# Optimization experiments

Measured on AMD Instinct MI355X. Metric: run time of the kernel, lower is better.

Reference implementation:

```python
import jax, jax.numpy as jnp
import numpy as np
from jax import lax

L = 25            # max_delay (250 // init_spike_step=10, odd)
SIG = 12.0        # max_delay // 2, frozen (requires_grad=False)
BN_EPS = 1e-5
EPS = 1e-7


def _dcls_kernel(W, P):
    # Gaussian interpolation of kernel_count=1 weights onto a dense kernel of size L.
    # W, P: (out, in). Returns (out, in, L).
    grid = jnp.arange(L, dtype=W.dtype) - L // 2          # (L,)
    K = jnp.exp(-0.5 * ((grid[None, None, :] - P[:, :, None]) / SIG) ** 2)
    K = K / (jnp.sum(K, axis=-1, keepdims=True) + EPS)    # normalize over kernel taps
    return W[:, :, None] * K


def _dcls_conv(x_tbc, W, P):
    # x_tbc: (T, B, Cin) -> causal dilated-kernel conv over time -> (T, B, Cout)
    kernel = _dcls_kernel(W, P)                           # (Cout, Cin, L)
    xb = jnp.transpose(x_tbc, (1, 2, 0))                  # (B, Cin, T)
    xb = jnp.pad(xb, ((0, 0), (0, 0), (L - 1, 0)))        # left (causal) padding
    y = lax.conv_general_dilated(xb, kernel, window_strides=(1,), padding='VALID',
                                 dimension_numbers=('NCH', 'OIH', 'NCH'))
    return jnp.transpose(y, (2, 0, 1))                    # (T, B, Cout)


def _bn(x_tbc, gamma, beta):
    # BatchNorm1d with step_mode='m': stats over merged (T, B) per channel.
    mean = jnp.mean(x_tbc, axis=(0, 1))
    var = jnp.var(x_tbc, axis=(0, 1))
    xhat = (x_tbc - mean) * lax.rsqrt(var + BN_EPS)
    return gamma * xhat + beta


def setup_inputs() -> dict:
    key = jax.random.key(0)
    ks = jax.random.split(key, 8)
    B, T, C = 128, 100, 700
    x = jax.random.uniform(ks[0], (B, T, C), dtype=jnp.float32)
    pmax = float(L // 2)
    W1 = jax.random.normal(ks[1], (256, 700), jnp.float32) * (1.0 / np.sqrt(700))
    P1 = jax.random.uniform(ks[2], (256, 700), jnp.float32, minval=-pmax, maxval=pmax)
    W2 = jax.random.normal(ks[3], (256, 256), jnp.float32) * (1.0 / np.sqrt(256))
    P2 = jax.random.uniform(ks[4], (256, 256), jnp.float32, minval=-pmax, maxval=pmax)
    W3 = jax.random.normal(ks[5], (20, 256), jnp.float32) * (1.0 / np.sqrt(256))
    P3 = jax.random.uniform(ks[6], (20, 256), jnp.float32, minval=-pmax, maxval=pmax)
    return {
        'x': x, 'W1': W1, 'P1': P1, 'W2': W2, 'P2': P2, 'W3': W3, 'P3': P3,
        'gamma1': jnp.ones((256,), jnp.float32), 'beta1': jnp.zeros((256,), jnp.float32),
        'gamma2': jnp.ones((256,), jnp.float32), 'beta2': jnp.zeros((256,), jnp.float32),
    }


def reference(x, W1, P1, W2, P2, W3, P3, gamma1, beta1, gamma2, beta2):
    h = jnp.transpose(x, (1, 0, 2))            # (T, B, C)
    h = _dcls_conv(h, W1, P1)                  # (T, B, 256)
    h = jax.nn.relu(_bn(h, gamma1, beta1))     # dropout = identity (eval)
    h = _dcls_conv(h, W2, P2)                  # (T, B, 256)
    h = jax.nn.relu(_bn(h, gamma2, beta2))
    h = _dcls_conv(h, W3, P3)                  # (T, B, 20)
    return jnp.sum(jax.nn.softmax(h, axis=2), axis=0)   # (B, 20)
```

## Files before the change

kernel.cpp:

```cpp
#include <hip/hip_runtime.h>
#include <stdint.h>


#define T_LEN 100
#define B_SZ  128
#define M_ROWS 12800
#define R_RANK 5
#define K_FIR 512

typedef __bf16 v8bf __attribute__((ext_vector_type(8)));
typedef float  v4f  __attribute__((ext_vector_type(4)));
typedef unsigned int uint32;
typedef unsigned short ushort_t;

struct PhiT { float v[25][R_RANK]; };
constexpr double cexp_(double x) {
  double s = 1.0, t = 1.0;
  for (int n = 1; n < 30; ++n) { t = t * x / n; s += t; }
  return s;
}
constexpr PhiT make_phi() {
  PhiT P{};
  for (int tau = 0; tau < 25; ++tau) {
    double u = (tau - 12) / 12.0;
    double g = cexp_(-0.5 * u * u);
    double T0 = 1.0, T1 = u;
    P.v[tau][0] = (float)(g * T0);
    P.v[tau][1] = (float)(g * T1);
    for (int r = 2; r < R_RANK; ++r) {
      double T2 = 2.0 * u * T1 - T0;
      P.v[tau][r] = (float)(g * T2);
      T0 = T1; T1 = T2;
    }
  }
  return P;
}
constexpr PhiT PHI = make_phi();

__device__ __forceinline__ void gl_lds16(const void* g, void* l) {
  __builtin_amdgcn_global_load_lds(
      (const __attribute__((address_space(1))) char*)g,
      (__attribute__((address_space(3))) char*)l, 16, 0, 0);
}

__device__ __forceinline__ void build_wr_body(
    const float* __restrict__ W, const float* __restrict__ P,
    __bf16* __restrict__ Wr, int CIN, int CINP, int COUT, int COUTP,
    int NRANK_OUT, int o) {
  for (int i = threadIdx.x; i < CINP; i += blockDim.x) {
    bool valid = (o < COUT) && (i < CIN);
    float w = valid ? W[(size_t)o * CIN + i] : 0.f;
    float p = valid ? P[(size_t)o * CIN + i] : 0.f;
    float S = 0.f;
#pragma unroll
    for (int l = 0; l < 25; ++l) {
      float d = ((float)(l - 12) - p) * (1.f / 12.f);
      S += expf(-0.5f * d * d);
    }
    float v = p * (1.f / 12.f);
    float g = w * expf(-0.5f * v * v) / (S + 1e-7f);
    float h = 0.5f * v, hh = h * h;
    float Ir[R_RANK];
    float pw = 1.f;
#pragma unroll
    for (int r = 0; r < R_RANK; ++r) {
      float term = pw, sum = pw;
#pragma unroll
      for (int m = 1; m <= 6; ++m) {
        term *= hh / (float)(m * (m + r));
        sum += term;
      }
      Ir[r] = sum;
      pw *= h / (float)(r + 1);
    }
    for (int r = 0; r < NRANK_OUT; ++r) {
      float c = (r < R_RANK) ? g * ((r == 0) ? 1.f : 2.f) * Ir[r] : 0.f;
      Wr[((size_t)r * COUTP + o) * CINP + i] = (__bf16)c;
    }
  }
}

__global__ void setup_all(const float* __restrict__ x,
                          const float* __restrict__ W1, const float* __restrict__ P1,
                          const float* __restrict__ W2, const float* __restrict__ P2,
                          const float* __restrict__ W3, const float* __restrict__ P3,
                          __bf16* __restrict__ Xb, __bf16* __restrict__ Wr1,
                          __bf16* __restrict__ Wr2, __bf16* __restrict__ Wr3,
                          __bf16* __restrict__ Af, float* __restrict__ stats) {
  int blk = blockIdx.x;
  if (blk < 256) { build_wr_body(W1, P1, Wr1, 700, 704, 256, 256, 5, blk); return; }
  blk -= 256;
  if (blk < 256) { build_wr_body(W2, P2, Wr2, 256, 256, 256, 256, 5, blk); return; }
  blk -= 256;
  if (blk < 32) { build_wr_body(W3, P3, Wr3, 256, 256, 20, 32, 6, blk); return; }
  blk -= 32;
  if (blk < 224) {
    int idx = blk * 256 + threadIdx.x;
    int t = idx >> 9, k = idx & 511;
    float v = 0.f;
    if (t < 100 && k < 500) {
      int r = k / 100, s = k - r * 100;
      int tau = s - t + 24;
      if (tau >= 0 && tau < 25) v = PHI.v[tau][r];
    }
    Af[idx] = (__bf16)v;
    return;
  }
  blk -= 224;
  if (blk < 12800) {
    int t = blk >> 7, b = blk & 127;
    const float* src = x + ((size_t)b * T_LEN + t) * 700;
    __bf16* dst = Xb + (size_t)blk * 704;
    for (int c = threadIdx.x; c < 704; c += 256) dst[c] = (c < 700) ? (__bf16)src[c] : (__bf16)0.f;
    return;
  }
  blk -= 12800;
  if (blk == 0) {
    for (int i = threadIdx.x; i < 1024; i += 256) stats[i] = 0.f;
  }
}

template <int CINP, int BLK_N, int WROWS, int WCOLS, int CO_SH>
__global__ __launch_bounds__(256, 2)
void gemm_rk64(const __bf16* __restrict__ A, const __bf16* __restrict__ Bm,
               __bf16* __restrict__ Z) {
  constexpr int COUTP = 1 << CO_SH;
  constexpr int WM = 128 / WROWS;
  constexpr int WN = BLK_N / WCOLS;
  constexpr int RM = WM / 16;
  constexpr int RN = WN / 16;
  __shared__ __align__(16) __bf16 sA[128 * 64];
  __shared__ __align__(16) __bf16 sB[BLK_N * 64];

  const int tid = threadIdx.x;
  const int w = tid >> 6, lane = tid & 63;
  const int q = lane >> 4, ln = lane & 15;
  const int wrow = w / WCOLS, wcol = w % WCOLS;
  const int srow8 = lane >> 3;
  const int s8 = lane & 7;

  const int t0 = blockIdx.x;
  const int oc = blockIdx.y * BLK_N;
  const __bf16* Abase = A + (size_t)t0 * 128 * CINP;
  const __bf16* Bbase = Bm + (size_t)oc * CINP;

  v4f acc[RM][RN];
#pragma unroll
  for (int a = 0; a < RM; ++a)
#pragma unroll
    for (int b = 0; b < RN; ++b) acc[a][b] = v4f{0.f, 0.f, 0.f, 0.f};

  for (int ic = 0; ic < CINP; ic += 64) {
    for (int j = w; j < 16; j += 4) {
      int m = j * 8 + srow8;
      int g = s8 ^ (m & 7);
      gl_lds16(Abase + (size_t)m * CINP + ic + g * 8, &sA[j * 512]);
    }
    for (int j = w; j < BLK_N / 8; j += 4) {
      int n = j * 8 + srow8;
      int g = s8 ^ (n & 7);
      gl_lds16(Bbase + (size_t)n * CINP + ic + g * 8, &sB[j * 512]);
    }
    __syncthreads();

#pragma unroll
    for (int s = 0; s < 2; ++s) {
      v8bf af[RM], bfr[RN];
#pragma unroll
      for (int a = 0; a < RM; ++a) {
        int m = wrow * WM + a * 16 + ln;
        af[a] = *(const v8bf*)&sA[m * 64 + ((((s << 2) | q) ^ (m & 7)) * 8)];
      }
#pragma unroll
      for (int b = 0; b < RN; ++b) {
        int n = wcol * WN + b * 16 + ln;
        bfr[b] = *(const v8bf*)&sB[n * 64 + ((((s << 2) | q) ^ (n & 7)) * 8)];
      }
#pragma unroll
      for (int a = 0; a < RM; ++a)
#pragma unroll
        for (int b = 0; b < RN; ++b)
          acc[a][b] = __builtin_amdgcn_mfma_f32_16x16x32_bf16(af[a], bfr[b], acc[a][b], 0, 0, 0);
    }
    __syncthreads();
  }

#pragma unroll
  for (int a = 0; a < RM; ++a) {
#pragma unroll
    for (int b = 0; b < RN; ++b) {
      int n = oc + wcol * WN + b * 16 + ln;
      int r = n >> CO_SH, o = n & (COUTP - 1);
#pragma unroll
      for (int rr = 0; rr < 4; ++rr) {
        int m = t0 * 128 + wrow * WM + a * 16 + q * 4 + rr;
        Z[((size_t)r * M_ROWS + m) * COUTP + o] = (__bf16)acc[a][b][rr];
      }
    }
  }
}

template <int COUTP, bool STATS, bool SOFTMAX>
__global__ __launch_bounds__(256, 2)
void fir_gemm64(const __bf16* __restrict__ Af, const __bf16* __restrict__ Z,
                __bf16* __restrict__ Yout, float* __restrict__ stats,
                float* __restrict__ outp, int N) {
  __shared__ __align__(16) unsigned char smem[26624];
  __bf16* sA = (__bf16*)smem;
  uint32* sBu = (uint32*)(smem + 14336);

  const int tid = threadIdx.x;
  const int w = tid >> 6, lane = tid & 63;
  const int q = lane >> 4, ln = lane & 15;
  const int srow8 = lane >> 3, s8 = lane & 7;
  const int kp = tid >> 3;
  const int noct = tid & 7;
  const int nb = blockIdx.x * 64;

  v4f acc[7];
#pragma unroll
  for (int a = 0; a < 7; ++a) acc[a] = v4f{0.f, 0.f, 0.f, 0.f};

  for (int kc = 0; kc < K_FIR; kc += 64) {
    for (int j = w; j < 14; j += 4) {
      int m = j * 8 + srow8;
      int g = s8 ^ (m & 7);
      gl_lds16(Af + (size_t)m * K_FIR + kc + g * 8, &sA[j * 512]);
    }
    const __bf16* zp = Z + (size_t)(kc + kp * 2) * N + nb + noct * 8;
    uint4 r0 = *(const uint4*)zp;
    uint4 r1 = *(const uint4*)(zp + N);
    const ushort_t* p0 = (const ushort_t*)&r0;
    const ushort_t* p1 = (const ushort_t*)&r1;
#pragma unroll
    for (int j = 0; j < 8; ++j) {
      uint32 val = (uint32)p0[j] | ((uint32)p1[j] << 16);
      sBu[(noct * 8 + j) * 35 + kp] = val;
    }
    __syncthreads();

#pragma unroll
    for (int s = 0; s < 2; ++s) {
      v8bf af[7];
#pragma unroll
      for (int a = 0; a < 7; ++a) {
        int m = a * 16 + ln;
        af[a] = *(const v8bf*)&sA[m * 64 + ((((s << 2) | q) ^ (m & 7)) * 8)];
      }
      int base = (w * 16 + ln) * 35 + s * 16 + q * 4;
      uint32 tmp[4] = {sBu[base], sBu[base + 1], sBu[base + 2], sBu[base + 3]};
      v8bf bfr = *(const v8bf*)tmp;
#pragma unroll
      for (int a = 0; a < 7; ++a)
        acc[a] = __builtin_amdgcn_mfma_f32_16x16x32_bf16(af[a], bfr, acc[a], 0, 0, 0);
    }
    __syncthreads();
  }

  int ng = nb + w * 16 + ln;
  if (!SOFTMAX) {
    float s = 0.f, ss = 0.f;
#pragma unroll
    for (int a = 0; a < 7; ++a) {
#pragma unroll
      for (int rr = 0; rr < 4; ++rr) {
        int t = a * 16 + q * 4 + rr;
        float v = acc[a][rr];
        if (t < 100) {
          Yout[(size_t)t * N + ng] = (__bf16)v;
          s += v; ss += v * v;
        }
      }
    }
    if (STATS) {
      s += __shfl_xor(s, 16); ss += __shfl_xor(ss, 16);
      s += __shfl_xor(s, 32); ss += __shfl_xor(ss, 32);
      if (q == 0) {
        int o = ng & (COUTP - 1);
        atomicAdd(&stats[o], s);
        atomicAdd(&stats[COUTP + o], ss);
      }
    }
  } else {
    float* smx = (float*)smem;
    float* lacc = (float*)(smem + 26000);
    int col = w * 16 + ln;
#pragma unroll
    for (int a = 0; a < 7; ++a) {
#pragma unroll
      for (int rr = 0; rr < 4; ++rr) {
        int t = a * 16 + q * 4 + rr;
        if (t < 100) smx[t * 65 + col] = acc[a][rr];
      }
    }
    if (tid < 64) lacc[tid & 63] = 0.f;
    __syncthreads();
    if (tid < 200) {
      int bl = tid / 100, t = tid - bl * 100;
      const float* rr = &smx[t * 65 + bl * 32];
      float v[20], m = -1e30f;
#pragma unroll
      for (int o = 0; o < 20; ++o) { v[o] = rr[o]; m = fmaxf(m, v[o]); }
      float sum = 0.f;
#pragma unroll
      for (int o = 0; o < 20; ++o) { v[o] = expf(v[o] - m); sum += v[o]; }
      float inv = 1.f / sum;
#pragma unroll
      for (int o = 0; o < 20; ++o) atomicAdd(&lacc[bl * 20 + o], v[o] * inv);
    }
    __syncthreads();
    if (tid < 40) {
      int bl = tid / 20, o = tid - bl * 20;
      int b = (nb >> 5) + bl;
      outp[b * 20 + o] = lacc[bl * 20 + o];
    }
  }
}

__global__ __launch_bounds__(256)
void bn_apply_relu8(const __bf16* __restrict__ h, const float* __restrict__ stats,
                    const float* __restrict__ gamma, const float* __restrict__ beta,
                    __bf16* __restrict__ hb) {
  int idx = blockIdx.x * 256 + threadIdx.x;
  int co = (idx & 31) * 8;
  size_t row = (size_t)(idx >> 5);
  const __bf16* src = h + row * 256 + co;
  __bf16* dst = hb + row * 256 + co;
  uint4 raw = *(const uint4*)src;
  const ushort_t* pr = (const ushort_t*)&raw;
  uint4 outv;
  ushort_t* po = (ushort_t*)&outv;
#pragma unroll
  for (int j = 0; j < 8; ++j) {
    int c = co + j;
    float mean = stats[c] * (1.f / 12800.f);
    float var = stats[256 + c] * (1.f / 12800.f) - mean * mean;
    float inv = rsqrtf(var + 1e-5f) * gamma[c];
    uint32 u = (uint32)pr[j] << 16;
    float xv; __builtin_memcpy(&xv, &u, 4);
    float v = (xv - mean) * inv + beta[c];
    v = fmaxf(v, 0.f);
    __bf16 bv = (__bf16)v;
    po[j] = *(const ushort_t*)&bv;
  }
  *(uint4*)dst = outv;
}


extern "C" void kernel_launch(void* const* d_in, const int* in_sizes, int n_in,
                              void* d_out, int out_size, void* d_ws, size_t ws_size,
                              hipStream_t stream) {
  const float* x  = (const float*)d_in[0];
  const float* W1 = (const float*)d_in[1];
  const float* P1 = (const float*)d_in[2];
  const float* W2 = (const float*)d_in[3];
  const float* P2 = (const float*)d_in[4];
  const float* W3 = (const float*)d_in[5];
  const float* P3 = (const float*)d_in[6];
  const float* g1 = (const float*)d_in[7];
  const float* b1 = (const float*)d_in[8];
  const float* g2 = (const float*)d_in[9];
  const float* b2 = (const float*)d_in[10];
  float* out = (float*)d_out;

  constexpr size_t XB_B  = (size_t)M_ROWS * 704 * 2;
  constexpr size_t Z_B   = (size_t)K_FIR * 32768 * 2;
  constexpr size_t Y12_B = (size_t)M_ROWS * 256 * 2;
  constexpr size_t H_B   = (size_t)M_ROWS * 256 * 2;
  constexpr size_t W1_B  = (size_t)5 * 256 * 704 * 2;
  constexpr size_t W2_B  = (size_t)5 * 256 * 256 * 2;
  constexpr size_t W3_B  = (size_t)6 * 32 * 256 * 2;
  constexpr size_t AF_B  = (size_t)112 * K_FIR * 2;
  constexpr size_t ST_B  = 4096;
  constexpr size_t TOTAL = XB_B + Z_B + Y12_B + H_B + W1_B + W2_B + W3_B + AF_B + ST_B;
  if (ws_size < TOTAL) return;

  char* ws = (char*)d_ws;
  size_t off = 0;
  __bf16* Xb   = (__bf16*)(ws + off); off += XB_B;
  __bf16* Zb   = (__bf16*)(ws + off); off += Z_B;
  __bf16* Yb   = (__bf16*)(ws + off); off += Y12_B;
  __bf16* Hb   = (__bf16*)(ws + off); off += H_B;
  __bf16* Wr1  = (__bf16*)(ws + off); off += W1_B;
  __bf16* Wr2  = (__bf16*)(ws + off); off += W2_B;
  __bf16* Wr3  = (__bf16*)(ws + off); off += W3_B;
  __bf16* Afir = (__bf16*)(ws + off); off += AF_B;
  float*  stats1 = (float*)(ws + off);
  float*  stats2 = stats1 + 512;

  setup_all<<<dim3(13569), 256, 0, stream>>>(x, W1, P1, W2, P2, W3, P3,
                                             Xb, Wr1, Wr2, Wr3, Afir, stats1);

  gemm_rk64<704, 128, 2, 2, 8><<<dim3(100, 10), 256, 0, stream>>>(Xb, Wr1, Zb);
  fir_gemm64<256, true, false><<<dim3(512), 256, 0, stream>>>(Afir, Zb, Yb, stats1, nullptr, 32768);
  bn_apply_relu8<<<dim3(1600), 256, 0, stream>>>(Yb, stats1, g1, b1, Hb);

  gemm_rk64<256, 128, 2, 2, 8><<<dim3(100, 10), 256, 0, stream>>>(Hb, Wr2, Zb);
  fir_gemm64<256, true, false><<<dim3(512), 256, 0, stream>>>(Afir, Zb, Yb, stats2, nullptr, 32768);
  bn_apply_relu8<<<dim3(1600), 256, 0, stream>>>(Yb, stats2, g2, b2, Hb);

  gemm_rk64<256, 64, 2, 2, 5><<<dim3(100, 3), 256, 0, stream>>>(Hb, Wr3, Zb);
  fir_gemm64<32, false, true><<<dim3(64), 256, 0, stream>>>(Afir, Zb, nullptr, nullptr, out, 4096);
}
```

Baseline: 212.0 us.

## Cut low-rank delay basis to rank four and fuse BN+ReLU into GEMM loads

Shrinks the Chebyshev-Gaussian low-rank expansion of the delay kernel from five to four basis terms. This reduces the GEMM output width, the intermediate Z buffer and the FIR contraction length (K from 512 to 448). It also removes the separate BatchNorm+ReLU kernels: the following GEMM now applies per-channel scale/shift and ReLU while staging A tiles into shared memory. Dropping a rank lowers the accuracy of the kernel approximation. The fused path swaps async global-to-LDS copies for register loads plus ALU work.

```diff
diff --git a/kernel.cpp b/kernel.cpp
--- a/kernel.cpp
+++ b/kernel.cpp
@@ -5,8 +5,8 @@
 #define T_LEN 100
 #define B_SZ  128
 #define M_ROWS 12800
-#define R_RANK 5
-#define K_FIR 512
+#define R_RANK 4
+#define K_FIR 448
 
 typedef __bf16 v8bf __attribute__((ext_vector_type(8)));
 typedef float  v4f  __attribute__((ext_vector_type(4)));
@@ -45,8 +45,7 @@
 
 __device__ __forceinline__ void build_wr_body(
     const float* __restrict__ W, const float* __restrict__ P,
-    __bf16* __restrict__ Wr, int CIN, int CINP, int COUT, int COUTP,
-    int NRANK_OUT, int o) {
+    __bf16* __restrict__ Wr, int CIN, int CINP, int COUT, int COUTP, int o) {
   for (int i = threadIdx.x; i < CINP; i += blockDim.x) {
     bool valid = (o < COUT) && (i < CIN);
     float w = valid ? W[(size_t)o * CIN + i] : 0.f;
@@ -60,7 +59,6 @@
     float v = p * (1.f / 12.f);
     float g = w * expf(-0.5f * v * v) / (S + 1e-7f);
     float h = 0.5f * v, hh = h * h;
-    float Ir[R_RANK];
     float pw = 1.f;
 #pragma unroll
     for (int r = 0; r < R_RANK; ++r) {
@@ -70,12 +68,9 @@
         term *= hh / (float)(m * (m + r));
         sum += term;
       }
-      Ir[r] = sum;
+      float c = g * ((r == 0) ? 1.f : 2.f) * sum;
+      Wr[((size_t)r * COUTP + o) * CINP + i] = (__bf16)c;
       pw *= h / (float)(r + 1);
-    }
-    for (int r = 0; r < NRANK_OUT; ++r) {
-      float c = (r < R_RANK) ? g * ((r == 0) ? 1.f : 2.f) * Ir[r] : 0.f;
-      Wr[((size_t)r * COUTP + o) * CINP + i] = (__bf16)c;
     }
   }
 }
@@ -88,25 +83,27 @@
                           __bf16* __restrict__ Wr2, __bf16* __restrict__ Wr3,
                           __bf16* __restrict__ Af, float* __restrict__ stats) {
   int blk = blockIdx.x;
-  if (blk < 256) { build_wr_body(W1, P1, Wr1, 700, 704, 256, 256, 5, blk); return; }
+  if (blk < 256) { build_wr_body(W1, P1, Wr1, 700, 704, 256, 256, blk); return; }
   blk -= 256;
-  if (blk < 256) { build_wr_body(W2, P2, Wr2, 256, 256, 256, 256, 5, blk); return; }
+  if (blk < 256) { build_wr_body(W2, P2, Wr2, 256, 256, 256, 256, blk); return; }
   blk -= 256;
-  if (blk < 32) { build_wr_body(W3, P3, Wr3, 256, 256, 20, 32, 6, blk); return; }
+  if (blk < 32) { build_wr_body(W3, P3, Wr3, 256, 256, 20, 32, blk); return; }
   blk -= 32;
-  if (blk < 224) {
+  if (blk < 196) {
     int idx = blk * 256 + threadIdx.x;
-    int t = idx >> 9, k = idx & 511;
-    float v = 0.f;
-    if (t < 100 && k < 500) {
-      int r = k / 100, s = k - r * 100;
-      int tau = s - t + 24;
-      if (tau >= 0 && tau < 25) v = PHI.v[tau][r];
-    }
-    Af[idx] = (__bf16)v;
+    if (idx < 112 * 448) {
+      int t = idx / 448, k = idx - t * 448;
+      float v = 0.f;
+      if (t < 100 && k < 400) {
+        int r = k / 100, s = k - r * 100;
+        int tau = s - t + 24;
+        if (tau >= 0 && tau < 25) v = PHI.v[tau][r];
+      }
+      Af[idx] = (__bf16)v;
+    }
     return;
   }
-  blk -= 224;
+  blk -= 196;
   if (blk < 12800) {
     int t = blk >> 7, b = blk & 127;
     const float* src = x + ((size_t)b * T_LEN + t) * 700;
@@ -120,10 +117,12 @@
   }
 }
 
-template <int CINP, int BLK_N, int WROWS, int WCOLS, int CO_SH>
+template <int CINP, int BLK_N, int WROWS, int WCOLS, int CO_SH, bool BN>
 __global__ __launch_bounds__(256, 2)
 void gemm_rk64(const __bf16* __restrict__ A, const __bf16* __restrict__ Bm,
-               __bf16* __restrict__ Z) {
+               __bf16* __restrict__ Z,
+               const float* __restrict__ stats, const float* __restrict__ gamma,
+               const float* __restrict__ beta) {
   constexpr int COUTP = 1 << CO_SH;
   constexpr int WM = 128 / WROWS;
   constexpr int WN = BLK_N / WCOLS;
@@ -131,6 +130,8 @@
   constexpr int RN = WN / 16;
   __shared__ __align__(16) __bf16 sA[128 * 64];
   __shared__ __align__(16) __bf16 sB[BLK_N * 64];
+  __shared__ float sScale[BN ? 256 : 1];
+  __shared__ float sShift[BN ? 256 : 1];
 
   const int tid = threadIdx.x;
   const int w = tid >> 6, lane = tid & 63;
@@ -138,12 +139,23 @@
   const int wrow = w / WCOLS, wcol = w % WCOLS;
   const int srow8 = lane >> 3;
   const int s8 = lane & 7;
+  const int g_lane = s8 ^ srow8;
 
   const int t0 = blockIdx.x;
   const int oc = blockIdx.y * BLK_N;
   const __bf16* Abase = A + (size_t)t0 * 128 * CINP;
   const __bf16* Bbase = Bm + (size_t)oc * CINP;
 
+  if (BN) {
+    int c = tid;
+    float mean = stats[c] * (1.f / 12800.f);
+    float var = stats[256 + c] * (1.f / 12800.f) - mean * mean;
+    float sc = rsqrtf(var + 1e-5f) * gamma[c];
+    sScale[c] = sc;
+    sShift[c] = beta[c] - mean * sc;
+    __syncthreads();
+  }
+
   v4f acc[RM][RN];
 #pragma unroll
   for (int a = 0; a < RM; ++a)
@@ -151,10 +163,35 @@
     for (int b = 0; b < RN; ++b) acc[a][b] = v4f{0.f, 0.f, 0.f, 0.f};
 
   for (int ic = 0; ic < CINP; ic += 64) {
-    for (int j = w; j < 16; j += 4) {
-      int m = j * 8 + srow8;
-      int g = s8 ^ (m & 7);
-      gl_lds16(Abase + (size_t)m * CINP + ic + g * 8, &sA[j * 512]);
+    if (!BN) {
+      for (int j = w; j < 16; j += 4) {
+        int m = j * 8 + srow8;
+        int g = s8 ^ (m & 7);
+        gl_lds16(Abase + (size_t)m * CINP + ic + g * 8, &sA[j * 512]);
+      }
+    } else {
+      float scl[8], sht[8];
+#pragma unroll
+      for (int jj = 0; jj < 8; ++jj) {
+        scl[jj] = sScale[ic + g_lane * 8 + jj];
+        sht[jj] = sShift[ic + g_lane * 8 + jj];
+      }
+      for (int j = w; j < 16; j += 4) {
+        int m = j * 8 + srow8;
+        uint4 raw = *(const uint4*)(Abase + (size_t)m * CINP + ic + g_lane * 8);
+        const ushort_t* pr = (const ushort_t*)&raw;
+        uint4 outv;
+        ushort_t* po = (ushort_t*)&outv;
+#pragma unroll
+        for (int jj = 0; jj < 8; ++jj) {
+          uint32 u = (uint32)pr[jj] << 16;
+          float yv; __builtin_memcpy(&yv, &u, 4);
+          float vv = fmaxf(yv * scl[jj] + sht[jj], 0.f);
+          __bf16 bv = (__bf16)vv;
+          po[jj] = *(const ushort_t*)&bv;
+        }
+        *(uint4*)((char*)sA + (size_t)j * 1024 + (size_t)lane * 16) = outv;
+      }
     }
     for (int j = w; j < BLK_N / 8; j += 4) {
       int n = j * 8 + srow8;
@@ -315,35 +352,6 @@
       outp[b * 20 + o] = lacc[bl * 20 + o];
     }
   }
-}
-
-__global__ __launch_bounds__(256)
-void bn_apply_relu8(const __bf16* __restrict__ h, const float* __restrict__ stats,
-                    const float* __restrict__ gamma, const float* __restrict__ beta,
-                    __bf16* __restrict__ hb) {
-  int idx = blockIdx.x * 256 + threadIdx.x;
-  int co = (idx & 31) * 8;
-  size_t row = (size_t)(idx >> 5);
-  const __bf16* src = h + row * 256 + co;
-  __bf16* dst = hb + row * 256 + co;
-  uint4 raw = *(const uint4*)src;
-  const ushort_t* pr = (const ushort_t*)&raw;
-  uint4 outv;
-  ushort_t* po = (ushort_t*)&outv;
-#pragma unroll
-  for (int j = 0; j < 8; ++j) {
-    int c = co + j;
-    float mean = stats[c] * (1.f / 12800.f);
-    float var = stats[256 + c] * (1.f / 12800.f) - mean * mean;
-    float inv = rsqrtf(var + 1e-5f) * gamma[c];
-    uint32 u = (uint32)pr[j] << 16;
-    float xv; __builtin_memcpy(&xv, &u, 4);
-    float v = (xv - mean) * inv + beta[c];
-    v = fmaxf(v, 0.f);
-    __bf16 bv = (__bf16)v;
-    po[j] = *(const ushort_t*)&bv;
-  }
-  *(uint4*)dst = outv;
 }
 
 
@@ -366,13 +374,12 @@
   constexpr size_t XB_B  = (size_t)M_ROWS * 704 * 2;
   constexpr size_t Z_B   = (size_t)K_FIR * 32768 * 2;
   constexpr size_t Y12_B = (size_t)M_ROWS * 256 * 2;
-  constexpr size_t H_B   = (size_t)M_ROWS * 256 * 2;
-  constexpr size_t W1_B  = (size_t)5 * 256 * 704 * 2;
-  constexpr size_t W2_B  = (size_t)5 * 256 * 256 * 2;
-  constexpr size_t W3_B  = (size_t)6 * 32 * 256 * 2;
+  constexpr size_t W1_B  = (size_t)R_RANK * 256 * 704 * 2;
+  constexpr size_t W2_B  = (size_t)R_RANK * 256 * 256 * 2;
+  constexpr size_t W3_B  = (size_t)R_RANK * 32 * 256 * 2;
   constexpr size_t AF_B  = (size_t)112 * K_FIR * 2;
   constexpr size_t ST_B  = 4096;
-  constexpr size_t TOTAL = XB_B + Z_B + Y12_B + H_B + W1_B + W2_B + W3_B + AF_B + ST_B;
+  constexpr size_t TOTAL = XB_B + Z_B + Y12_B + W1_B + W2_B + W3_B + AF_B + ST_B;
   if (ws_size < TOTAL) return;
 
   char* ws = (char*)d_ws;
@@ -380,7 +387,6 @@
   __bf16* Xb   = (__bf16*)(ws + off); off += XB_B;
   __bf16* Zb   = (__bf16*)(ws + off); off += Z_B;
   __bf16* Yb   = (__bf16*)(ws + off); off += Y12_B;
-  __bf16* Hb   = (__bf16*)(ws + off); off += H_B;
   __bf16* Wr1  = (__bf16*)(ws + off); off += W1_B;
   __bf16* Wr2  = (__bf16*)(ws + off); off += W2_B;
   __bf16* Wr3  = (__bf16*)(ws + off); off += W3_B;
@@ -388,17 +394,21 @@
   float*  stats1 = (float*)(ws + off);
   float*  stats2 = stats1 + 512;
 
-  setup_all<<<dim3(13569), 256, 0, stream>>>(x, W1, P1, W2, P2, W3, P3,
+  setup_all<<<dim3(13541), 256, 0, stream>>>(x, W1, P1, W2, P2, W3, P3,
                                              Xb, Wr1, Wr2, Wr3, Afir, stats1);
 
-  gemm_rk64<704, 128, 2, 2, 8><<<dim3(100, 10), 256, 0, stream>>>(Xb, Wr1, Zb);
-  fir_gemm64<256, true, false><<<dim3(512), 256, 0, stream>>>(Afir, Zb, Yb, stats1, nullptr, 32768);
-  bn_apply_relu8<<<dim3(1600), 256, 0, stream>>>(Yb, stats1, g1, b1, Hb);
-
-  gemm_rk64<256, 128, 2, 2, 8><<<dim3(100, 10), 256, 0, stream>>>(Hb, Wr2, Zb);
-  fir_gemm64<256, true, false><<<dim3(512), 256, 0, stream>>>(Afir, Zb, Yb, stats2, nullptr, 32768);
-  bn_apply_relu8<<<dim3(1600), 256, 0, stream>>>(Yb, stats2, g2, b2, Hb);
-
-  gemm_rk64<256, 64, 2, 2, 5><<<dim3(100, 3), 256, 0, stream>>>(Hb, Wr3, Zb);
-  fir_gemm64<32, false, true><<<dim3(64), 256, 0, stream>>>(Afir, Zb, nullptr, nullptr, out, 4096);
-}
+  gemm_rk64<704, 128, 2, 2, 8, false><<<dim3(100, 8), 256, 0, stream>>>(
+      Xb, Wr1, Zb, nullptr, nullptr, nullptr);
+  fir_gemm64<256, true, false><<<dim3(512), 256, 0, stream>>>(
+      Afir, Zb, Yb, stats1, nullptr, 32768);
+
+  gemm_rk64<256, 128, 2, 2, 8, true><<<dim3(100, 8), 256, 0, stream>>>(
+      Yb, Wr2, Zb, stats1, g1, b1);
+  fir_gemm64<256, true, false><<<dim3(512), 256, 0, stream>>>(
+      Afir, Zb, Yb, stats2, nullptr, 32768);
+
+  gemm_rk64<256, 64, 2, 2, 5, true><<<dim3(100, 2), 256, 0, stream>>>(
+      Yb, Wr3, Zb, stats2, g2, b2);
+  fir_gemm64<32, false, true><<<dim3(64), 256, 0, stream>>>(
+      Afir, Zb, nullptr, nullptr, out, 4096);
+}
```

New measurement: 209.8 us. No clear change (-1.0%).
